# Performance work log

Hardware: AMD Instinct MI355X
Metric: run time of the kernel (lower is better)

## Reference

```python
import jax, jax.numpy as jnp
import numpy as np

B, S, D = 4, 2048, 1024
H = 2 * D          # hidden_dim = 2*n_embd
A = H // 16        # adapt_dim = 128
E = 8              # num_experts
K = 2              # top-k within group
GS = 4             # group_size
G = E // GS        # num_groups


def _ln(x, g, b, eps=1e-5):
    m = x.mean(-1, keepdims=True)
    v = x.var(-1, keepdims=True)
    return (x - m) / jnp.sqrt(v + eps) * g + b


def setup_inputs() -> dict:
    key = jax.random.key(0)
    ks = jax.random.split(key, 12)
    s = 1.0 / np.sqrt(D)       # shared MLP init scale
    sa = s * 0.01              # adapt layers init scale
    se = 0.01 / np.sqrt(A)     # expert adapter init scale
    f32 = jnp.float32
    return {
        "x": jax.random.normal(ks[0], (B, S, D), f32),
        "W_up": jax.random.normal(ks[1], (H, D), f32) * s,
        "W_gate": jax.random.normal(ks[2], (H, D), f32) * s,
        "W_down": jax.random.normal(ks[3], (D, H), f32) * s,
        "W_pre": jax.random.normal(ks[4], (A, D), f32) * sa,
        "W_post": jax.random.normal(ks[5], (A, H), f32) * sa,
        "g_an": jnp.ones((A,), f32),
        "b_an": jnp.zeros((A,), f32),
        "W_aproj": jax.random.normal(ks[6], (H, A), f32) * sa,
        "W_eadapt": jax.random.normal(ks[7], (E, A, A), f32) * se,
        "g_e": jnp.ones((E, A), f32),
        "b_e": jnp.zeros((E, A), f32),
        "W_eproj": jax.random.normal(ks[8], (H, A), f32) * se,
        "W_oproj": jax.random.normal(ks[9], (D, H), f32) * se,
        "W_rg": jax.random.normal(ks[10], (G, D), f32) * 0.001,
        "W_re": jax.random.normal(ks[11], (GS, D), f32) * 0.001,
    }


def reference(x, W_up, W_gate, W_down, W_pre, W_post, g_an, b_an, W_aproj,
              W_eadapt, g_e, b_e, W_eproj, W_oproj, W_rg, W_re):
    Bs, Ss, Ds = x.shape
    N = Bs * Ss
    xf = x.reshape(N, Ds)

    # ---- HierarchicalRouter ----
    gl = xf @ W_rg.T                                   # [N, G]
    gp = jax.nn.softmax(gl, axis=-1)
    gw = gp.max(axis=-1)                               # top-1 group weight
    gi = gp.argmax(axis=-1)                            # top-1 group index
    ll = xf @ W_re.T                                   # [N, GS]
    lp = jax.nn.softmax(ll, axis=-1)
    lw, li = jax.lax.top_k(lp, K)                      # [N, K]
    eidx = gi[:, None] * GS + li                       # global expert ids
    lw = lw / (lw.sum(-1, keepdims=True) + 1e-7)
    fw = gw[:, None] * lw                              # final weights [N, K]
    dispatch = jnp.zeros((N, E), x.dtype).at[jnp.arange(N)[:, None], eidx].set(fw)
    load = dispatch.sum(0)
    target = load.sum() / E
    load_balance_loss = jnp.mean((load - target) ** 2)
    z_loss = jnp.mean(gl ** 2) + jnp.mean(ll ** 2)
    router_loss = 0.001 * (load_balance_loss + z_loss)

    # ---- SharedExpertMLP ----
    up = x @ W_up.T                                    # [B, S, H]
    gate = x @ W_gate.T
    hidden = jax.nn.silu(gate) * up
    pre = x @ W_pre.T                                  # [B, S, A]
    a_in = _ln(pre, g_an, b_an)
    a_out = _ln(hidden @ W_post.T, g_an, b_an)
    aw = jax.nn.silu(jnp.clip(jnp.einsum('bsa,bta->bst', a_in, a_out), -5.0, 5.0))
    adapt = jnp.einsum('bst,bta->bsa', aw, a_in) @ W_aproj.T  # [B, S, H]
    hidden = hidden + 0.1 * adapt
    shared = hidden @ W_down.T                         # [B, S, D]

    # ---- ExpertGroup (vectorized gather/MLP/scatter) ----
    # sum_i w_i * (shared + 0.1*contrib_i) = shared*sum(w) + 0.1*sum_i w_i*contrib_i
    w = dispatch.reshape(Bs, Ss, E)                    # dispatch weights
    he = jnp.einsum('bsa,eca->ebsc', pre, W_eadapt)    # [E, B, S, A]
    he = _ln(he, g_e[:, None, None, :], b_e[:, None, None, :])
    wh = jnp.einsum('ebsa,bse->bsa', he, w)            # weighted combine at adapt_dim
    contrib = (wh @ W_eproj.T) @ W_oproj.T             # [B, S, D]
    out = shared * w.sum(-1, keepdims=True) + 0.1 * contrib
    return out, router_loss
```

## Files before the change

### kernel.cpp

```cpp
#include <hip/hip_runtime.h>
#include <hip/hip_bf16.h>

typedef unsigned short u16;
typedef short bf16x8 __attribute__((ext_vector_type(8)));
typedef float f32x4 __attribute__((ext_vector_type(4)));

#define N_TOK 8192
#define DIM   1024
#define HID   2048
#define ADIM  128
#define SEQ   2048
#define LDP   2304

__device__ __forceinline__ u16 f2bf_bits(float f){
  unsigned u = __float_as_uint(f);
  unsigned r = (u + 0x7fffu + ((u >> 16) & 1u)) >> 16;
  return (u16)r;
}
__device__ __forceinline__ float bf2f(u16 v){ return __uint_as_float((unsigned)v << 16); }
__device__ __forceinline__ float siluf(float x){ return x / (1.f + __expf(-x)); }

__device__ __forceinline__ void gload16(const void* g, void* l){
  __builtin_amdgcn_global_load_lds((const __attribute__((address_space(1))) void*)g,
                                   (__attribute__((address_space(3))) void*)l, 16, 0, 0);
// ... 129 lines not shown
      acc[2][n] = __builtin_amdgcn_mfma_f32_16x16x32_bf16(a[2], b[n], acc[2][n], 0, 0, 0);
    asm volatile("s_waitcnt lgkmcnt(0)" ::: "memory"); SB0();
    #pragma unroll
    for (int n = 0; n < 4; n++)
      acc[3][n] = __builtin_amdgcn_mfma_f32_16x16x32_bf16(a[3], b[n], acc[3][n], 0, 0, 0);
    __builtin_amdgcn_s_setprio(0);
    __builtin_amdgcn_s_barrier();

    a[0] = AFRAG(4, 1); SB0();
    a[1] = AFRAG(5, 1); SB0();
    a[2] = AFRAG(6, 1); SB0();
    a[3] = AFRAG(7, 1);
    stage(Wgu, bcol, ktn, 1, pn, 16384);
    __builtin_amdgcn_s_barrier();
    asm volatile("s_waitcnt lgkmcnt(3)" ::: "memory"); SB0();
    __builtin_amdgcn_s_setprio(1);
    #pragma unroll
    for (int n = 0; n < 4; n++)
      acc[4][n] = __builtin_amdgcn_mfma_f32_16x16x32_bf16(a[0], b[n], acc[4][n], 0, 0, 0);
    asm volatile("s_waitcnt lgkmcnt(2)" ::: "memory"); SB0();
    #pragma unroll
    for (int n = 0; n < 4; n++)
      acc[5][n] = __builtin_amdgcn_mfma_f32_16x16x32_bf16(a[1], b[n], acc[5][n], 0, 0, 0);
    asm volatile("s_waitcnt lgkmcnt(1)" ::: "memory"); SB0();
    #pragma unroll
    for (int n = 0; n < 4; n++)
      acc[6][n] = __builtin_amdgcn_mfma_f32_16x16x32_bf16(a[2], b[n], acc[6][n], 0, 0, 0);
    asm volatile("s_waitcnt lgkmcnt(0)" ::: "memory"); SB0();
    #pragma unroll
    for (int n = 0; n < 4; n++)
      acc[7][n] = __builtin_amdgcn_mfma_f32_16x16x32_bf16(a[3], b[n], acc[7][n], 0, 0, 0);
    __builtin_amdgcn_s_setprio(0);
    asm volatile("s_waitcnt vmcnt(4)" ::: "memory");
    __builtin_amdgcn_s_barrier();
  }
#undef AFRAG
#undef BFRAG

  #pragma unroll
  for (int mf = 0; mf < 8; mf++)
    #pragma unroll
    for (int i = 0; i < 4; i++) {
      const long r = brow + wm * 128 + mf * 16 + (lane >> 4) * 4 + i;
      const float sw = sumw[r];
      #pragma unroll
      for (int q = 0; q < 2; q++) {
        const float g = acc[mf][2 * q][i], u = acc[mf][2 * q + 1][i];
        const int hcol = (bn * 8 + wn * 2 + q) * 16 + (lane & 15);
        hidP[r * LDP + hcol] = f2bf_bits(sw * (siluf(g) * u));
      }
    }
}

enum { EPI_BF16 = 0, EPI_SILU = 2 };

template<int EPI>
__global__ void __launch_bounds__(256, 2)
gemm_bt(const u16* __restrict__ Ag, const u16* __restrict__ Bg, int K, int lda, int ldb,
        long sAz, long sBz, long sOz, u16* __restrict__ bout, int ldo, int col0)
{
  __shared__ u16 lA[128 * 32];
  __shared__ u16 lB[128 * 32];
  const int tid = threadIdx.x, wave = tid >> 6, lane = tid & 63;
  const long brow = (long)blockIdx.y * 128, bcol = (long)blockIdx.x * 128;
  const u16* A = Ag + (long)blockIdx.z * sAz + brow * lda;
  const u16* B = Bg + (long)blockIdx.z * sBz + bcol * ldb;
  const int wr = (wave >> 1) * 64, wc = (wave & 1) * 64;

  f32x4 acc[4][4];
  #pragma unroll
  for (int m = 0; m < 4; m++)
    #pragma unroll
    for (int n = 0; n < 4; n++)
      #pragma unroll
      for (int i = 0; i < 4; i++) acc[m][n][i] = 0.f;

  const int sr = tid >> 2, sks = ((tid & 3) ^ ((tid >> 3) & 3)) * 8;
  const u16* gA = A + (long)sr * lda + sks;
  const u16* gB = B + (long)sr * ldb + sks;
  const long rA = (long)64 * lda, rB = (long)64 * ldb;
  u16* lA0 = &lA[wave * 512]; u16* lA1 = &lA[2048 + wave * 512];
  u16* lB0 = &lB[wave * 512]; u16* lB1 = &lB[2048 + wave * 512];
  const int frow = lane & 15;
  const int fks = ((lane >> 4) * 8) ^ (((lane >> 1) & 3) << 3);

  for (int kt = 0; kt < K; kt += 32) {
    gload16(gA, lA0); gload16(gA + rA, lA1);
    gload16(gB, lB0); gload16(gB + rB, lB1);
    gA += 32; gB += 32;
    asm volatile("s_waitcnt vmcnt(0)" ::: "memory");
    __syncthreads();
    bf16x8 af[4], bfv[4];
    #pragma unroll
    for (int m = 0; m < 4; m++) af[m] = *(const bf16x8*)&lA[(wr + m * 16 + frow) * 32 + fks];
    #pragma unroll
    for (int n = 0; n < 4; n++) bfv[n] = *(const bf16x8*)&lB[(wc + n * 16 + frow) * 32 + fks];
    #pragma unroll
    for (int m = 0; m < 4; m++)
      #pragma unroll
      for (int n = 0; n < 4; n++)
        acc[m][n] = __builtin_amdgcn_mfma_f32_16x16x32_bf16(af[m], bfv[n], acc[m][n], 0, 0, 0);
    __syncthreads();
  }

  const long r0 = brow + wr + ((lane >> 4) << 2);
  const long c0 = bcol + wc + (lane & 15);
  u16* O = bout + (long)blockIdx.z * sOz;
  #pragma unroll
  for (int m = 0; m < 4; m++) {
    #pragma unroll
    for (int i = 0; i < 4; i++) {
      long r = r0 + m * 16 + i;
      #pragma unroll
      for (int n = 0; n < 4; n++) {
        long c = c0 + n * 16;
        float v = acc[m][n][i];
        if constexpr (EPI == EPI_BF16) {
          O[r * ldo + col0 + c] = f2bf_bits(v);
        } else {
          v = fminf(5.f, fmaxf(-5.f, v));
          O[r * ldo + c] = f2bf_bits(siluf(v));
        }
      }
    }
  }
}

__global__ void __launch_bounds__(256, 2)
gemm_f32(const u16* __restrict__ Ag, const u16* __restrict__ Bg,
         float* __restrict__ out)
{
  __shared__ u16 lA[128 * 32];
  __shared__ u16 lB[128 * 32];
  const int tid = threadIdx.x, wave = tid >> 6, lane = tid & 63;
  const long brow = (long)blockIdx.y * 128, bcol = (long)blockIdx.x * 128;
  const int wr = (wave >> 1) * 64, wc = (wave & 1) * 64;

  f32x4 acc[4][4];
  #pragma unroll
  for (int m = 0; m < 4; m++)
    #pragma unroll
    for (int n = 0; n < 4; n++)
      #pragma unroll
      for (int i = 0; i < 4; i++) acc[m][n][i] = 0.f;

  const int sr = tid >> 2, sks = ((tid & 3) ^ ((tid >> 3) & 3)) * 8;
  const u16* gA = Ag + brow * LDP + (long)sr * LDP + sks;
  const u16* gB = Bg + bcol * LDP + (long)sr * LDP + sks;
  const long rA = (long)64 * LDP, rB = (long)64 * LDP;
  u16* lA0 = &lA[wave * 512]; u16* lA1 = &lA[2048 + wave * 512];
  u16* lB0 = &lB[wave * 512]; u16* lB1 = &lB[2048 + wave * 512];
  const int frow = lane & 15;
  const int fks = ((lane >> 4) * 8) ^ (((lane >> 1) & 3) << 3);

  for (int kt = 0; kt < LDP; kt += 32) {
    gload16(gA, lA0); gload16(gA + rA, lA1);
    gload16(gB, lB0); gload16(gB + rB, lB1);
    gA += 32; gB += 32;
    asm volatile("s_waitcnt vmcnt(0)" ::: "memory");
    __syncthreads();
    bf16x8 af[4], bfv[4];
    #pragma unroll
    for (int m = 0; m < 4; m++) af[m] = *(const bf16x8*)&lA[(wr + m * 16 + frow) * 32 + fks];
    #pragma unroll
    for (int n = 0; n < 4; n++) bfv[n] = *(const bf16x8*)&lB[(wc + n * 16 + frow) * 32 + fks];
    #pragma unroll
    for (int m = 0; m < 4; m++)
      #pragma unroll
      for (int n = 0; n < 4; n++)
        acc[m][n] = __builtin_amdgcn_mfma_f32_16x16x32_bf16(af[m], bfv[n], acc[m][n], 0, 0, 0);
    __syncthreads();
  }

  const long r0 = brow + wr + ((lane >> 4) << 2);
  const long c0 = bcol + wc + (lane & 15);
  #pragma unroll
  for (int m = 0; m < 4; m++)
    #pragma unroll
    for (int i = 0; i < 4; i++) {
      long r = r0 + m * 16 + i;
      #pragma unroll
      for (int n = 0; n < 4; n++)
        out[r * DIM + c0 + n * 16] = acc[m][n][i];
    }
}

__global__ void __launch_bounds__(256, 2)
gemm_split(const u16* __restrict__ Ag, const u16* __restrict__ Bg, int Ksub, int nsplit,
           int lda, int ldb, long sAz, long sBz, float* __restrict__ part)
{
  __shared__ u16 lA[128 * 32];
  __shared__ u16 lB[128 * 32];
  const int tid = threadIdx.x, wave = tid >> 6, lane = tid & 63;
  const int z = blockIdx.z, batch = z / nsplit, split = z % nsplit;
  const long brow = (long)blockIdx.y * 128;
  const int Mrows = gridDim.y * 128;
  const u16* A = Ag + (long)batch * sAz + brow * lda + (long)split * Ksub;
  const u16* B = Bg + (long)batch * sBz + (long)split * Ksub;
  const int wr = (wave >> 1) * 64, wc = (wave & 1) * 64;

  f32x4 acc[4][4];
  #pragma unroll
  for (int m = 0; m < 4; m++)
    #pragma unroll
    for (int n = 0; n < 4; n++)
      #pragma unroll
      for (int i = 0; i < 4; i++) acc[m][n][i] = 0.f;

  const int sr = tid >> 2, sks = ((tid & 3) ^ ((tid >> 3) & 3)) * 8;
  const u16* gA = A + (long)sr * lda + sks;
  const u16* gB = B + (long)sr * ldb + sks;
  const long rA = (long)64 * lda, rB = (long)64 * ldb;
  u16* lA0 = &lA[wave * 512]; u16* lA1 = &lA[2048 + wave * 512];
  u16* lB0 = &lB[wave * 512]; u16* lB1 = &lB[2048 + wave * 512];
  const int frow = lane & 15;
  const int fks = ((lane >> 4) * 8) ^ (((lane >> 1) & 3) << 3);

  for (int kt = 0; kt < Ksub; kt += 32) {
    gload16(gA, lA0); gload16(gA + rA, lA1);
    gload16(gB, lB0); gload16(gB + rB, lB1);
    gA += 32; gB += 32;
    asm volatile("s_waitcnt vmcnt(0)" ::: "memory");
    __syncthreads();
    bf16x8 af[4], bfv[4];
    #pragma unroll
    for (int m = 0; m < 4; m++) af[m] = *(const bf16x8*)&lA[(wr + m * 16 + frow) * 32 + fks];
    #pragma unroll
    for (int n = 0; n < 4; n++) bfv[n] = *(const bf16x8*)&lB[(wc + n * 16 + frow) * 32 + fks];
    #pragma unroll
    for (int m = 0; m < 4; m++)
      #pragma unroll
      for (int n = 0; n < 4; n++)
        acc[m][n] = __builtin_amdgcn_mfma_f32_16x16x32_bf16(af[m], bfv[n], acc[m][n], 0, 0, 0);
    __syncthreads();
  }

  float* po = part + (long)z * Mrows * 128;
  const long rr = brow + wr + ((lane >> 4) << 2);
  const int cc = wc + (lane & 15);
  #pragma unroll
  for (int m = 0; m < 4; m++)
    #pragma unroll
    for (int i = 0; i < 4; i++) {
      long r = rr + m * 16 + i;
      #pragma unroll
      for (int n = 0; n < 4; n++)
        po[r * 128 + cc + n * 16] = acc[m][n][i];
    }
}

__global__ void __launch_bounds__(256, 2)
gemm_split_q(const u16* __restrict__ A0, const u16* __restrict__ B0, int lda0,
             const u16* __restrict__ A1, const u16* __restrict__ B1, int lda1,
             float* __restrict__ part)
{
  __shared__ u16 lA[128 * 32];
  __shared__ u16 lB[128 * 32];
  const int tid = threadIdx.x, wave = tid >> 6, lane = tid & 63;
  const int z = blockIdx.z, sel = z >> 2, split = z & 3;
  const long brow = (long)blockIdx.y * 128;
  const int lda = sel ? lda1 : lda0;
  const u16* A = (sel ? A1 : A0) + brow * lda + (long)split * 512;
  const u16* B = (sel ? B1 : B0) + (long)split * 512;

  const int wr = (wave >> 1) * 64, wc = (wave & 1) * 64;
  f32x4 acc[4][4];
  #pragma unroll
  for (int m = 0; m < 4; m++)
    #pragma unroll
    for (int n = 0; n < 4; n++)
      #pragma unroll
      for (int i = 0; i < 4; i++) acc[m][n][i] = 0.f;

  const int sr = tid >> 2, sks = ((tid & 3) ^ ((tid >> 3) & 3)) * 8;
  const u16* gA = A + (long)sr * lda + sks;
  const u16* gB = B + (long)sr * HID + sks;
  const long rA = (long)64 * lda, rB = (long)64 * HID;
  u16* lA0 = &lA[wave * 512]; u16* lA1 = &lA[2048 + wave * 512];
  u16* lB0 = &lB[wave * 512]; u16* lB1 = &lB[2048 + wave * 512];
  const int frow = lane & 15;
  const int fks = ((lane >> 4) * 8) ^ (((lane >> 1) & 3) << 3);

  for (int kt = 0; kt < 512; kt += 32) {
    gload16(gA, lA0); gload16(gA + rA, lA1);
    gload16(gB, lB0); gload16(gB + rB, lB1);
    gA += 32; gB += 32;
    asm volatile("s_waitcnt vmcnt(0)" ::: "memory");
    __syncthreads();
    bf16x8 af[4], bfv[4];
    #pragma unroll
    for (int m = 0; m < 4; m++) af[m] = *(const bf16x8*)&lA[(wr + m * 16 + frow) * 32 + fks];
    #pragma unroll
    for (int n = 0; n < 4; n++) bfv[n] = *(const bf16x8*)&lB[(wc + n * 16 + frow) * 32 + fks];
    #pragma unroll
    for (int m = 0; m < 4; m++)
      #pragma unroll
      for (int n = 0; n < 4; n++)
        acc[m][n] = __builtin_amdgcn_mfma_f32_16x16x32_bf16(af[m], bfv[n], acc[m][n], 0, 0, 0);
    __syncthreads();
  }

  float* po = part + (long)z * 131072;
  const long rr = brow + wr + ((lane >> 4) << 2);
  const int cc = wc + (lane & 15);
  #pragma unroll
  for (int m = 0; m < 4; m++)
    #pragma unroll
    for (int i = 0; i < 4; i++) {
      long r = rr + m * 16 + i;
      #pragma unroll
      for (int n = 0; n < 4; n++)
        po[r * 128 + cc + n * 16] = acc[m][n][i];
    }
}

__global__ void __launch_bounds__(256)
prep_all(const float* __restrict__ x, const float* __restrict__ Wrg,
         const float* __restrict__ Wre, float* __restrict__ sumw,
         float* __restrict__ fwv, int* __restrict__ eidxv,
         float* __restrict__ stats, u16* __restrict__ xb,
         const float* __restrict__ Wg, const float* __restrict__ Wu,
         const float* __restrict__ Wd, const float* __restrict__ Wo,
         const float* __restrict__ Wpost, const float* __restrict__ Wpre,
         const float* __restrict__ Wead,
         u16* __restrict__ Wgu, u16* __restrict__ WdQ,
         u16* __restrict__ Wob, u16* __restrict__ Wpostb,
         u16* __restrict__ Wpreb, u16* __restrict__ Weadb,
         const float* __restrict__ Wa, const float* __restrict__ We,
         u16* __restrict__ Ta, u16* __restrict__ Te)
{
  __shared__ float lst[10];
  const int blk = blockIdx.x;
  if (blk < 512) {
    if (threadIdx.x < 10) lst[threadIdx.x] = 0.f;
    __syncthreads();
    const int wave = threadIdx.x >> 6, lane = threadIdx.x & 63;
    const float4* wg0 = (const float4*)Wrg;
    const float4* wg1 = (const float4*)(Wrg + 1024);
    const float4* we0 = (const float4*)Wre;
    const float4* we1 = (const float4*)(Wre + 1024);
    const float4* we2 = (const float4*)(Wre + 2048);
    const float4* we3 = (const float4*)(Wre + 3072);
    for (int t = 0; t < 4; t++) {
      const long n = (long)blk * 16 + wave * 4 + t;
      const float4* xr = (const float4*)(x + n * 1024);
      float d0 = 0, d1 = 0, t0 = 0, t1 = 0, t2 = 0, t3 = 0;
      #pragma unroll
      for (int j = 0; j < 4; j++) {
        int id = j * 64 + lane;
        float4 xv = xr[id];
        ushort4 xc;
        xc.x = f2bf_bits(xv.x); xc.y = f2bf_bits(xv.y);
        xc.z = f2bf_bits(xv.z); xc.w = f2bf_bits(xv.w);
        *(ushort4*)(xb + n * 1024 + id * 4) = xc;
        float4 a;
        a = wg0[id]; d0 += xv.x * a.x + xv.y * a.y + xv.z * a.z + xv.w * a.w;
        a = wg1[id]; d1 += xv.x * a.x + xv.y * a.y + xv.z * a.z + xv.w * a.w;
        a = we0[id]; t0 += xv.x * a.x + xv.y * a.y + xv.z * a.z + xv.w * a.w;
        a = we1[id]; t1 += xv.x * a.x + xv.y * a.y + xv.z * a.z + xv.w * a.w;
        a = we2[id]; t2 += xv.x * a.x + xv.y * a.y + xv.z * a.z + xv.w * a.w;
        a = we3[id]; t3 += xv.x * a.x + xv.y * a.y + xv.z * a.z + xv.w * a.w;
      }
      #pragma unroll
      for (int o = 32; o; o >>= 1) {
        d0 += __shfl_xor(d0, o); d1 += __shfl_xor(d1, o);
        t0 += __shfl_xor(t0, o); t1 += __shfl_xor(t1, o);
// ... 19 lines not shown
        for (int i = 1; i < 4; i++) if (p[i] > p[i1]) i1 = i;
        int i2 = (i1 == 0) ? 1 : 0;
        #pragma unroll
        for (int i = 0; i < 4; i++) if (i != i1 && p[i] > p[i2]) i2 = i;
        float s2 = p[i1] + p[i2];
        float invs = 1.f / (s2 + 1e-7f);
        float f1 = gw * p[i1] * invs, f2 = gw * p[i2] * invs;
        int ea = gi * 4 + i1, eb = gi * 4 + i2;
        sumw[n] = f1 + f2;
        fwv[2 * n] = f1; fwv[2 * n + 1] = f2;
        eidxv[2 * n] = ea; eidxv[2 * n + 1] = eb;
        atomicAdd(&lst[ea], f1);
        atomicAdd(&lst[eb], f2);
        atomicAdd(&lst[8], d0 * d0 + d1 * d1);
        atomicAdd(&lst[9], t0 * t0 + t1 * t1 + t2 * t2 + t3 * t3);
      }
    }
    __syncthreads();
    if (threadIdx.x < 10) atomicAdd(&stats[threadIdx.x], lst[threadIdx.x]);
  } else if (blk < 4864) {
    long i = ((long)(blk - 512) * 256 + threadIdx.x) * 8;
    const float* s; u16* d; long so, doff;
    if (i < 4194304) {
      long rp = i >> 10, c = i & 1023;
      long i32 = rp >> 5, wi = rp & 31;
      s = (wi < 16) ? Wg : Wu;
      so = (i32 * 16 + (wi & 15)) * 1024 + c;
      d = Wgu; doff = i;
    } else if (i < 6291456) {
      long j = i - 4194304;
      long r = j >> 11, c = j & 2047;
      s = Wd; so = j;
      d = WdQ; doff = r * LDP + c;
    } else if (i < 8388608) { s = Wo;    so = i - 6291456; d = Wob;    doff = so; }
    else if (i < 8650752)   { s = Wpost; so = i - 8388608; d = Wpostb; doff = so; }
    else if (i < 8781824)   { s = Wpre;  so = i - 8650752; d = Wpreb;  doff = so; }
    else                    { s = Wead;  so = i - 8781824; d = Weadb;  doff = so; }
    float4 v0 = *(const float4*)(s + so), v1 = *(const float4*)(s + so + 4);
    ushort4 p, q;
    p.x = f2bf_bits(v0.x); p.y = f2bf_bits(v0.y); p.z = f2bf_bits(v0.z); p.w = f2bf_bits(v0.w);
    q.x = f2bf_bits(v1.x); q.y = f2bf_bits(v1.y); q.z = f2bf_bits(v1.z); q.w = f2bf_bits(v1.w);
    *(ushort4*)(d + doff) = p;
    *(ushort4*)(d + doff + 4) = q;
  } else {
    int bid = blk - 4864;
    const float* src = (bid < 1024) ? Wa : We;
    u16* dst = (bid < 1024) ? Ta : Te;
    int idx = (bid & 1023) * 256 + threadIdx.x;
    int c = idx >> 11, r = idx & 2047;
    dst[idx] = f2bf_bits(src[(long)r * 128 + c]);
  }
}

__global__ void reduce_q(const float* __restrict__ part, u16* __restrict__ WdQ)
{
  int idx = blockIdx.x * 256 + threadIdx.x;
  int r = idx >> 8, c = idx & 255;
  const float* p = part + ((c < 128) ? 0 : 524288) + (long)r * 128 + (c & 127);
  float a = p[0] + p[131072] + p[262144] + p[393216];
  WdQ[(long)r * LDP + 2048 + c] = f2bf_bits(a);
}

__global__ void __launch_bounds__(256)
ln_rows_part(const float* __restrict__ part, int nsplit,
             const float* __restrict__ g, const float* __restrict__ b,
             const float* __restrict__ sumw,
             u16* __restrict__ out, u16* __restrict__ outT, u16* __restrict__ rawout)
{
  int wave = threadIdx.x >> 6, lane = threadIdx.x & 63;
  long n = (long)blockIdx.x * 4 + wave;
  long base = n * 128;
  float x0 = 0.f, x1 = 0.f;
  for (int s = 0; s < nsplit; s++) {
    x0 += part[(long)s * (N_TOK * ADIM) + base + lane];
    x1 += part[(long)s * (N_TOK * ADIM) + base + 64 + lane];
  }
  if (sumw) { float inv = 1.f / sumw[n]; x0 *= inv; x1 *= inv; }
  float s2 = x0 + x1, q = x0 * x0 + x1 * x1;
  #pragma unroll
  for (int o = 32; o; o >>= 1) { s2 += __shfl_xor(s2, o); q += __shfl_xor(q, o); }
  float m = s2 * (1.f / 128.f);
  float var = q * (1.f / 128.f) - m * m;
  float inv = rsqrtf(var + 1e-5f);
  float y0 = (x0 - m) * inv * g[lane] + b[lane];
  float y1 = (x1 - m) * inv * g[lane + 64] + b[lane + 64];
  out[base + lane] = f2bf_bits(y0);
  out[base + 64 + lane] = f2bf_bits(y1);
  if (outT) {
    long bb = n >> 11, ss = n & 2047;
    outT[(bb * 128 + lane) * 2048 + ss] = f2bf_bits(y0);
    outT[(bb * 128 + lane + 64) * 2048 + ss] = f2bf_bits(y1);
  }
  if (rawout) {
    rawout[base + lane] = f2bf_bits(x0);
    rawout[base + 64 + lane] = f2bf_bits(x1);
  }
}

__global__ void reduce_part_p1(const float* __restrict__ part,
                               const float* __restrict__ sumw, u16* __restrict__ hidP)
{
  int idx = blockIdx.x * 256 + threadIdx.x;
  int n = idx >> 5, c4 = (idx & 31) * 4;
  int batch = n >> 11, r = n & 2047;
  float4 a = {0.f, 0.f, 0.f, 0.f};
  #pragma unroll
  for (int s = 0; s < 4; s++) {
    float4 v = *(const float4*)(part + (((long)(batch * 4 + s) * 2048 + r) << 7) + c4);
    a.x += v.x; a.y += v.y; a.z += v.z; a.w += v.w;
  }
  float rs = 0.1f * sumw[n];
  ushort4 o;
  o.x = f2bf_bits(rs * a.x); o.y = f2bf_bits(rs * a.y);
  o.z = f2bf_bits(rs * a.z); o.w = f2bf_bits(rs * a.w);
  *(ushort4*)(hidP + (long)n * LDP + 2048 + c4) = o;
}

__global__ void init_stats(float* stats){ if (threadIdx.x < 16) stats[threadIdx.x] = 0.f; }

__global__ void finalize_loss(const float* __restrict__ stats, float* __restrict__ out)
{
  float tot = 0;
  #pragma unroll
  for (int e = 0; e < 8; e++) tot += stats[e];
  float target = tot * 0.125f;
  float lb = 0;
  #pragma unroll
  for (int e = 0; e < 8; e++) { float d = stats[e] - target; lb += d * d; }
  lb *= 0.125f;
  float z = stats[8] * (1.f / (8192.f * 2.f)) + stats[9] * (1.f / (8192.f * 4.f));
  out[0] = 0.001f * (lb + z);
}

__global__ void __launch_bounds__(256)
ln_combine(const u16* __restrict__ he, const int* __restrict__ eidxv,
           const float* __restrict__ fwv, const float* __restrict__ g_e,
           const float* __restrict__ b_e, u16* __restrict__ hidP)
{
  const int wave = threadIdx.x >> 6, lane = threadIdx.x & 63;
  const long n = (long)blockIdx.x * 4 + wave;
  float o0 = 0.f, o1 = 0.f;
  #pragma unroll
  for (int k = 0; k < 2; k++) {
    const int e = eidxv[2 * n + k];
    const float w = fwv[2 * n + k];
    const u16* row = he + ((long)e * N_TOK + n) * 128;
    float h0 = bf2f(row[lane]), h1 = bf2f(row[lane + 64]);
    float s = h0 + h1, q = h0 * h0 + h1 * h1;
    #pragma unroll
    for (int o = 32; o; o >>= 1) { s += __shfl_xor(s, o); q += __shfl_xor(q, o); }
    float m = s * (1.f / 128.f);
    float var = q * (1.f / 128.f) - m * m;
    float inv = rsqrtf(var + 1e-5f);
    o0 += w * ((h0 - m) * inv * g_e[e * 128 + lane] + b_e[e * 128 + lane]);
    o1 += w * ((h1 - m) * inv * g_e[e * 128 + lane + 64] + b_e[e * 128 + lane + 64]);
  }
  hidP[n * LDP + 2176 + lane] = f2bf_bits(0.1f * o0);
  hidP[n * LDP + 2176 + 64 + lane] = f2bf_bits(0.1f * o1);
}

extern "C" void kernel_launch(void* const* d_in, const int* in_sizes, int n_in,
                              void* d_out, int out_size, void* d_ws, size_t ws_size,
                              hipStream_t stream)
{
  (void)in_sizes; (void)n_in; (void)out_size; (void)ws_size;
  const float* x       = (const float*)d_in[0];
  const float* W_up    = (const float*)d_in[1];
  const float* W_gate  = (const float*)d_in[2];
  const float* W_down  = (const float*)d_in[3];
  const float* W_pre   = (const float*)d_in[4];
  const float* W_post  = (const float*)d_in[5];
  const float* g_an    = (const float*)d_in[6];
  const float* b_an    = (const float*)d_in[7];
  const float* W_aproj = (const float*)d_in[8];
  const float* W_ead   = (const float*)d_in[9];
  const float* g_e     = (const float*)d_in[10];
  const float* b_e     = (const float*)d_in[11];
  const float* W_eproj = (const float*)d_in[12];
  const float* W_oproj = (const float*)d_in[13];
  const float* W_rg    = (const float*)d_in[14];
  const float* W_re    = (const float*)d_in[15];
  float* out = (float*)d_out;

  char* base = (char*)d_ws; size_t off = 0;
  auto alloc = [&](size_t bytes) -> void* {
    void* p = base + off; off = (off + bytes + 255) & ~(size_t)255; return p;
  };
  u16*   xb     = (u16*)  alloc((size_t)N_TOK * DIM * 2);
  u16*   Wgu    = (u16*)  alloc((size_t)2 * HID * DIM * 2);
  u16*   WdQ    = (u16*)  alloc((size_t)DIM * LDP * 2);
  u16*   Wob    = (u16*)  alloc((size_t)DIM * HID * 2);
  u16*   Wpostb = (u16*)  alloc((size_t)ADIM * HID * 2);
  u16*   Wpreb  = (u16*)  alloc((size_t)ADIM * DIM * 2);
  u16*   WaTb   = (u16*)  alloc((size_t)ADIM * HID * 2);
  u16*   WeTb   = (u16*)  alloc((size_t)ADIM * HID * 2);
  u16*   Weadb  = (u16*)  alloc((size_t)8 * ADIM * ADIM * 2);
  u16*   hidP   = (u16*)  alloc((size_t)N_TOK * LDP * 2);
  u16*   heb    = (u16*)  alloc((size_t)8 * N_TOK * ADIM * 2);
  float* part   = (float*)heb;
  u16*   preb   = (u16*)  alloc((size_t)N_TOK * ADIM * 2);
  u16*   a_in   = (u16*)  alloc((size_t)N_TOK * ADIM * 2);
  u16*   a_inT  = (u16*)  alloc((size_t)N_TOK * ADIM * 2);
  u16*   a_out  = (u16*)  alloc((size_t)N_TOK * ADIM * 2);
  float* sumw   = (float*)alloc((size_t)N_TOK * 4);
  float* fwv    = (float*)alloc((size_t)N_TOK * 2 * 4);
  int*   eidxv  = (int*)  alloc((size_t)N_TOK * 2 * 4);
  float* stats  = (float*)alloc(64);
  u16* aw = (u16*)d_out;

  hipFuncSetAttribute((const void*)gemm_gu256,
                      hipFuncAttributeMaxDynamicSharedMemorySize, 131072);

  init_stats<<<1, 64, 0, stream>>>(stats);

  prep_all<<<6912, 256, 0, stream>>>(x, W_rg, W_re, sumw, fwv, eidxv, stats, xb,
                                     W_gate, W_up, W_down, W_oproj, W_post, W_pre,
                                     W_ead, Wgu, WdQ, Wob, Wpostb, Wpreb, Weadb,
                                     W_aproj, W_eproj, WaTb, WeTb);

  gemm_split_q<<<dim3(1, 8, 8), 256, 0, stream>>>(WdQ, WaTb, LDP, Wob, WeTb, HID, part);
  reduce_q<<<1024, 256, 0, stream>>>(part, WdQ);

  gemm_gu256<<<512, 512, 131072, stream>>>(xb, Wgu, sumw, hidP);

  gemm_split<<<dim3(1, 64, 4), 256, 0, stream>>>(xb, Wpreb, 256, 4, DIM, DIM, 0, 0, part);
  ln_rows_part<<<2048, 256, 0, stream>>>(part, 4, g_an, b_an, nullptr, a_in, a_inT, preb);

  gemm_bt<EPI_BF16><<<dim3(1, 64, 8), 256, 0, stream>>>(preb, Weadb, ADIM, ADIM, ADIM,
      0, (long)ADIM * ADIM, (long)N_TOK * ADIM, heb, ADIM, 0);
  ln_combine<<<2048, 256, 0, stream>>>(heb, eidxv, fwv, g_e, b_e, hidP);

  gemm_split<<<dim3(1, 64, 4), 256, 0, stream>>>(hidP, Wpostb, 512, 4, LDP, HID, 0, 0, part);
  ln_rows_part<<<2048, 256, 0, stream>>>(part, 4, g_an, b_an, sumw, a_out, nullptr, nullptr);

  gemm_bt<EPI_SILU><<<dim3(16, 16, 4), 256, 0, stream>>>(a_in, a_out, ADIM, ADIM, ADIM,
      (long)SEQ * ADIM, (long)SEQ * ADIM, (long)SEQ * SEQ, aw, SEQ, 0);

  gemm_split<<<dim3(1, 16, 16), 256, 0, stream>>>(aw, a_inT, 512, 4, SEQ, SEQ,
      (long)SEQ * SEQ, (long)ADIM * SEQ, part);
  reduce_part_p1<<<1024, 256, 0, stream>>>(part, sumw, hidP);

  gemm_f32<<<dim3(8, 64, 1), 256, 0, stream>>>(hidP, WdQ, out);

  finalize_loss<<<1, 1, 0, stream>>>(stats, out + (size_t)N_TOK * DIM);
}
```

Before: 269.9 us.

## Merge independent GEMM and layernorm launches into fewer combined kernels

Small independent GEMMs and their follow-up reductions and layernorms now share launches, dispatched by block-index ranges. The pre-projection GEMM runs with the weight-fold GEMM, the expert-adapter GEMM with the post-projection GEMM, and their layernorm or reduce steps are paired the same way. Loss finalisation moves into the last GEMM, and the stats init becomes a memset. This cuts launch count and tail underutilisation from small grids, at the cost of reusing the output buffer as scratch for partial sums.

```diff
diff --git a/kernel.cpp b/kernel.cpp
--- a/kernel.cpp
+++ b/kernel.cpp
@@ -205,29 +205,12 @@
     }
 }
 
-enum { EPI_BF16 = 0, EPI_SILU = 2 };
-
-template<int EPI>
-__global__ void __launch_bounds__(256, 2)
-gemm_bt(const u16* __restrict__ Ag, const u16* __restrict__ Bg, int K, int lda, int ldb,
-        long sAz, long sBz, long sOz, u16* __restrict__ bout, int ldo, int col0)
-{
-  __shared__ u16 lA[128 * 32];
-  __shared__ u16 lB[128 * 32];
+__device__ __forceinline__ void kloop128(const u16* __restrict__ A, const u16* __restrict__ B,
+                                         int lda, int ldb, int K,
+                                         u16* lA, u16* lB, f32x4 (&acc)[4][4])
+{
   const int tid = threadIdx.x, wave = tid >> 6, lane = tid & 63;
-  const long brow = (long)blockIdx.y * 128, bcol = (long)blockIdx.x * 128;
-  const u16* A = Ag + (long)blockIdx.z * sAz + brow * lda;
-  const u16* B = Bg + (long)blockIdx.z * sBz + bcol * ldb;
   const int wr = (wave >> 1) * 64, wc = (wave & 1) * 64;
-
-  f32x4 acc[4][4];
-  #pragma unroll
-  for (int m = 0; m < 4; m++)
-    #pragma unroll
-    for (int n = 0; n < 4; n++)
-      #pragma unroll
-      for (int i = 0; i < 4; i++) acc[m][n][i] = 0.f;
-
   const int sr = tid >> 2, sks = ((tid & 3) ^ ((tid >> 3) & 3)) * 8;
   const u16* gA = A + (long)sr * lda + sks;
   const u16* gB = B + (long)sr * ldb + sks;
@@ -255,76 +238,193 @@
         acc[m][n] = __builtin_amdgcn_mfma_f32_16x16x32_bf16(af[m], bfv[n], acc[m][n], 0, 0, 0);
     __syncthreads();
   }
-
+}
+
+__device__ __forceinline__ void acc_zero(f32x4 (&acc)[4][4]){
+  #pragma unroll
+  for (int m = 0; m < 4; m++)
+    #pragma unroll
+    for (int n = 0; n < 4; n++)
+      #pragma unroll
+      for (int i = 0; i < 4; i++) acc[m][n][i] = 0.f;
+}
+
+__global__ void __launch_bounds__(256, 2)
+gemm_silu(const u16* __restrict__ Ag, const u16* __restrict__ Bg,
+          u16* __restrict__ bout)
+{
+  __shared__ u16 lA[4096];
+  __shared__ u16 lB[4096];
+  const int wave = threadIdx.x >> 6, lane = threadIdx.x & 63;
+  const long brow = (long)blockIdx.y * 128, bcol = (long)blockIdx.x * 128;
+  const u16* A = Ag + (long)blockIdx.z * (SEQ * ADIM) + brow * ADIM;
+  const u16* B = Bg + (long)blockIdx.z * (SEQ * ADIM) + bcol * ADIM;
+  f32x4 acc[4][4]; acc_zero(acc);
+  kloop128(A, B, ADIM, ADIM, ADIM, lA, lB, acc);
+  const int wr = (wave >> 1) * 64, wc = (wave & 1) * 64;
   const long r0 = brow + wr + ((lane >> 4) << 2);
   const long c0 = bcol + wc + (lane & 15);
-  u16* O = bout + (long)blockIdx.z * sOz;
+  u16* O = bout + (long)blockIdx.z * ((long)SEQ * SEQ);
   #pragma unroll
-  for (int m = 0; m < 4; m++) {
+  for (int m = 0; m < 4; m++)
     #pragma unroll
     for (int i = 0; i < 4; i++) {
       long r = r0 + m * 16 + i;
       #pragma unroll
       for (int n = 0; n < 4; n++) {
-        long c = c0 + n * 16;
         float v = acc[m][n][i];
-        if constexpr (EPI == EPI_BF16) {
-          O[r * ldo + col0 + c] = f2bf_bits(v);
-        } else {
-          v = fminf(5.f, fmaxf(-5.f, v));
-          O[r * ldo + c] = f2bf_bits(siluf(v));
-        }
-      }
-    }
+        v = fminf(5.f, fmaxf(-5.f, v));
+        O[r * SEQ + c0 + n * 16] = f2bf_bits(siluf(v));
+      }
+    }
+}
+
+__global__ void __launch_bounds__(256, 2)
+gemm_split_p1(const u16* __restrict__ aw, const u16* __restrict__ a_inT,
+              float* __restrict__ part)
+{
+  __shared__ u16 lA[4096];
+  __shared__ u16 lB[4096];
+  const int wave = threadIdx.x >> 6, lane = threadIdx.x & 63;
+  const int z = blockIdx.z, batch = z >> 2, split = z & 3;
+  const long brow = (long)blockIdx.y * 128;
+  const u16* A = aw + (long)batch * SEQ * SEQ + brow * SEQ + (long)split * 512;
+  const u16* B = a_inT + (long)batch * ADIM * SEQ + (long)split * 512;
+  f32x4 acc[4][4]; acc_zero(acc);
+  kloop128(A, B, SEQ, SEQ, 512, lA, lB, acc);
+  float* po = part + (long)z * (SEQ * ADIM);
+  const int wr = (wave >> 1) * 64, wc = (wave & 1) * 64;
+  const long rr = brow + wr + ((lane >> 4) << 2);
+  const int cc = wc + (lane & 15);
+  #pragma unroll
+  for (int m = 0; m < 4; m++)
+    #pragma unroll
+    for (int i = 0; i < 4; i++) {
+      long r = rr + m * 16 + i;
+      #pragma unroll
+      for (int n = 0; n < 4; n++)
+        po[r * 128 + cc + n * 16] = acc[m][n][i];
+    }
+}
+
+__global__ void __launch_bounds__(256, 2)
+split_pq(const u16* __restrict__ xb, const u16* __restrict__ Wpreb,
+         const u16* __restrict__ WdQ, const u16* __restrict__ WaTb,
+         const u16* __restrict__ Wob, const u16* __restrict__ WeTb,
+         float* __restrict__ part, float* __restrict__ qpart)
+{
+  __shared__ u16 lA[4096];
+  __shared__ u16 lB[4096];
+  const int blk = blockIdx.x;
+  const int wave = threadIdx.x >> 6, lane = threadIdx.x & 63;
+  f32x4 acc[4][4]; acc_zero(acc);
+  const int wr = (wave >> 1) * 64, wc = (wave & 1) * 64;
+
+  if (blk < 256) {
+    const int y = blk & 63, z = blk >> 6;
+    const long brow = (long)y * 128;
+    const u16* A = xb + brow * DIM + (long)z * 256;
+    const u16* B = Wpreb + (long)z * 256;
+    kloop128(A, B, DIM, DIM, 256, lA, lB, acc);
+    float* po = part + (long)z * (N_TOK * ADIM);
+    const long rr = brow + wr + ((lane >> 4) << 2);
+    const int cc = wc + (lane & 15);
+    #pragma unroll
+    for (int m = 0; m < 4; m++)
+      #pragma unroll
+      for (int i = 0; i < 4; i++) {
+        long r = rr + m * 16 + i;
+        #pragma unroll
+        for (int n = 0; n < 4; n++)
+          po[r * 128 + cc + n * 16] = acc[m][n][i];
+      }
+  } else {
+    const int q = blk - 256;
+    const int y = q & 7, z = q >> 3;
+    const int sel = z >> 2, split = z & 3;
+    const long brow = (long)y * 128;
+    const int lda = sel ? HID : LDP;
+    const u16* A = (sel ? Wob : WdQ) + brow * lda + (long)split * 512;
+    const u16* B = (sel ? WeTb : WaTb) + (long)split * 512;
+    kloop128(A, B, lda, HID, 512, lA, lB, acc);
+    float* po = qpart + (long)z * 131072;
+    const long rr = brow + wr + ((lane >> 4) << 2);
+    const int cc = wc + (lane & 15);
+    #pragma unroll
+    for (int m = 0; m < 4; m++)
+      #pragma unroll
+      for (int i = 0; i < 4; i++) {
+        long r = rr + m * 16 + i;
+        #pragma unroll
+        for (int n = 0; n < 4; n++)
+          po[r * 128 + cc + n * 16] = acc[m][n][i];
+      }
+  }
+}
+
+__global__ void __launch_bounds__(256, 2)
+he_postf(const u16* __restrict__ preb, const u16* __restrict__ Weadb,
+         u16* __restrict__ heb, const u16* __restrict__ hidP,
+         const u16* __restrict__ Wpostb, float* __restrict__ postfp)
+{
+  __shared__ u16 lA[4096];
+  __shared__ u16 lB[4096];
+  const int blk = blockIdx.x;
+  const int wave = threadIdx.x >> 6, lane = threadIdx.x & 63;
+  f32x4 acc[4][4]; acc_zero(acc);
+  const int wr = (wave >> 1) * 64, wc = (wave & 1) * 64;
+
+  if (blk < 512) {
+    const int y = blk & 63, e = blk >> 6;
+    const long brow = (long)y * 128;
+    const u16* A = preb + brow * ADIM;
+    const u16* B = Weadb + (long)e * ADIM * ADIM;
+    kloop128(A, B, ADIM, ADIM, ADIM, lA, lB, acc);
+    u16* O = heb + (long)e * N_TOK * ADIM;
+    const long r0 = brow + wr + ((lane >> 4) << 2);
+    const long c0 = wc + (lane & 15);
+    #pragma unroll
+    for (int m = 0; m < 4; m++)
+      #pragma unroll
+      for (int i = 0; i < 4; i++) {
+        long r = r0 + m * 16 + i;
+        #pragma unroll
+        for (int n = 0; n < 4; n++)
+          O[r * ADIM + c0 + n * 16] = f2bf_bits(acc[m][n][i]);
+      }
+  } else {
+    const int q = blk - 512;
+    const int y = q & 63, z = q >> 6;
+    const long brow = (long)y * 128;
+    const u16* A = hidP + brow * LDP + (long)z * 512;
+    const u16* B = Wpostb + (long)z * 512;
+    kloop128(A, B, LDP, HID, 512, lA, lB, acc);
+    float* po = postfp + (long)z * (N_TOK * ADIM);
+    const long rr = brow + wr + ((lane >> 4) << 2);
+    const int cc = wc + (lane & 15);
+    #pragma unroll
+    for (int m = 0; m < 4; m++)
+      #pragma unroll
+      for (int i = 0; i < 4; i++) {
+        long r = rr + m * 16 + i;
+        #pragma unroll
+        for (int n = 0; n < 4; n++)
+          po[r * 128 + cc + n * 16] = acc[m][n][i];
+      }
   }
 }
 
 __global__ void __launch_bounds__(256, 2)
 gemm_f32(const u16* __restrict__ Ag, const u16* __restrict__ Bg,
-         float* __restrict__ out)
-{
-  __shared__ u16 lA[128 * 32];
-  __shared__ u16 lB[128 * 32];
-  const int tid = threadIdx.x, wave = tid >> 6, lane = tid & 63;
+         const float* __restrict__ stats, float* __restrict__ out)
+{
+  __shared__ u16 lA[4096];
+  __shared__ u16 lB[4096];
+  const int wave = threadIdx.x >> 6, lane = threadIdx.x & 63;
   const long brow = (long)blockIdx.y * 128, bcol = (long)blockIdx.x * 128;
+  f32x4 acc[4][4]; acc_zero(acc);
+  kloop128(Ag + brow * LDP, Bg + bcol * LDP, LDP, LDP, LDP, lA, lB, acc);
   const int wr = (wave >> 1) * 64, wc = (wave & 1) * 64;
-
-  f32x4 acc[4][4];
-  #pragma unroll
-  for (int m = 0; m < 4; m++)
-    #pragma unroll
-    for (int n = 0; n < 4; n++)
-      #pragma unroll
-      for (int i = 0; i < 4; i++) acc[m][n][i] = 0.f;
-
-  const int sr = tid >> 2, sks = ((tid & 3) ^ ((tid >> 3) & 3)) * 8;
-  const u16* gA = Ag + brow * LDP + (long)sr * LDP + sks;
-  const u16* gB = Bg + bcol * LDP + (long)sr * LDP + sks;
-  const long rA = (long)64 * LDP, rB = (long)64 * LDP;
-  u16* lA0 = &lA[wave * 512]; u16* lA1 = &lA[2048 + wave * 512];
-  u16* lB0 = &lB[wave * 512]; u16* lB1 = &lB[2048 + wave * 512];
-  const int frow = lane & 15;
-  const int fks = ((lane >> 4) * 8) ^ (((lane >> 1) & 3) << 3);
-
-  for (int kt = 0; kt < LDP; kt += 32) {
-    gload16(gA, lA0); gload16(gA + rA, lA1);
-    gload16(gB, lB0); gload16(gB + rB, lB1);
-    gA += 32; gB += 32;
-    asm volatile("s_waitcnt vmcnt(0)" ::: "memory");
-    __syncthreads();
-    bf16x8 af[4], bfv[4];
-    #pragma unroll
-    for (int m = 0; m < 4; m++) af[m] = *(const bf16x8*)&lA[(wr + m * 16 + frow) * 32 + fks];
-    #pragma unroll
-    for (int n = 0; n < 4; n++) bfv[n] = *(const bf16x8*)&lB[(wc + n * 16 + frow) * 32 + fks];
-    #pragma unroll
-    for (int m = 0; m < 4; m++)
-      #pragma unroll
-      for (int n = 0; n < 4; n++)
-        acc[m][n] = __builtin_amdgcn_mfma_f32_16x16x32_bf16(af[m], bfv[n], acc[m][n], 0, 0, 0);
-    __syncthreads();
-  }
-
   const long r0 = brow + wr + ((lane >> 4) << 2);
   const long c0 = bcol + wc + (lane & 15);
   #pragma unroll
@@ -336,135 +436,18 @@
       for (int n = 0; n < 4; n++)
         out[r * DIM + c0 + n * 16] = acc[m][n][i];
     }
-}
-
-__global__ void __launch_bounds__(256, 2)
-gemm_split(const u16* __restrict__ Ag, const u16* __restrict__ Bg, int Ksub, int nsplit,
-           int lda, int ldb, long sAz, long sBz, float* __restrict__ part)
-{
-  __shared__ u16 lA[128 * 32];
-  __shared__ u16 lB[128 * 32];
-  const int tid = threadIdx.x, wave = tid >> 6, lane = tid & 63;
-  const int z = blockIdx.z, batch = z / nsplit, split = z % nsplit;
-  const long brow = (long)blockIdx.y * 128;
-  const int Mrows = gridDim.y * 128;
-  const u16* A = Ag + (long)batch * sAz + brow * lda + (long)split * Ksub;
-  const u16* B = Bg + (long)batch * sBz + (long)split * Ksub;
-  const int wr = (wave >> 1) * 64, wc = (wave & 1) * 64;
-
-  f32x4 acc[4][4];
-  #pragma unroll
-  for (int m = 0; m < 4; m++)
-    #pragma unroll
-    for (int n = 0; n < 4; n++)
-      #pragma unroll
-      for (int i = 0; i < 4; i++) acc[m][n][i] = 0.f;
-
-  const int sr = tid >> 2, sks = ((tid & 3) ^ ((tid >> 3) & 3)) * 8;
-  const u16* gA = A + (long)sr * lda + sks;
-  const u16* gB = B + (long)sr * ldb + sks;
-  const long rA = (long)64 * lda, rB = (long)64 * ldb;
-  u16* lA0 = &lA[wave * 512]; u16* lA1 = &lA[2048 + wave * 512];
-  u16* lB0 = &lB[wave * 512]; u16* lB1 = &lB[2048 + wave * 512];
-  const int frow = lane & 15;
-  const int fks = ((lane >> 4) * 8) ^ (((lane >> 1) & 3) << 3);
-
-  for (int kt = 0; kt < Ksub; kt += 32) {
-    gload16(gA, lA0); gload16(gA + rA, lA1);
-    gload16(gB, lB0); gload16(gB + rB, lB1);
-    gA += 32; gB += 32;
-    asm volatile("s_waitcnt vmcnt(0)" ::: "memory");
-    __syncthreads();
-    bf16x8 af[4], bfv[4];
-    #pragma unroll
-    for (int m = 0; m < 4; m++) af[m] = *(const bf16x8*)&lA[(wr + m * 16 + frow) * 32 + fks];
-    #pragma unroll
-    for (int n = 0; n < 4; n++) bfv[n] = *(const bf16x8*)&lB[(wc + n * 16 + frow) * 32 + fks];
-    #pragma unroll
-    for (int m = 0; m < 4; m++)
-      #pragma unroll
-      for (int n = 0; n < 4; n++)
-        acc[m][n] = __builtin_amdgcn_mfma_f32_16x16x32_bf16(af[m], bfv[n], acc[m][n], 0, 0, 0);
-    __syncthreads();
-  }
-
-  float* po = part + (long)z * Mrows * 128;
-  const long rr = brow + wr + ((lane >> 4) << 2);
-  const int cc = wc + (lane & 15);
-  #pragma unroll
-  for (int m = 0; m < 4; m++)
-    #pragma unroll
-    for (int i = 0; i < 4; i++) {
-      long r = rr + m * 16 + i;
-      #pragma unroll
-      for (int n = 0; n < 4; n++)
-        po[r * 128 + cc + n * 16] = acc[m][n][i];
-    }
-}
-
-__global__ void __launch_bounds__(256, 2)
-gemm_split_q(const u16* __restrict__ A0, const u16* __restrict__ B0, int lda0,
-             const u16* __restrict__ A1, const u16* __restrict__ B1, int lda1,
-             float* __restrict__ part)
-{
-  __shared__ u16 lA[128 * 32];
-  __shared__ u16 lB[128 * 32];
-  const int tid = threadIdx.x, wave = tid >> 6, lane = tid & 63;
-  const int z = blockIdx.z, sel = z >> 2, split = z & 3;
-  const long brow = (long)blockIdx.y * 128;
-  const int lda = sel ? lda1 : lda0;
-  const u16* A = (sel ? A1 : A0) + brow * lda + (long)split * 512;
-  const u16* B = (sel ? B1 : B0) + (long)split * 512;
-
-  const int wr = (wave >> 1) * 64, wc = (wave & 1) * 64;
-  f32x4 acc[4][4];
-  #pragma unroll
-  for (int m = 0; m < 4; m++)
-    #pragma unroll
-    for (int n = 0; n < 4; n++)
-      #pragma unroll
-      for (int i = 0; i < 4; i++) acc[m][n][i] = 0.f;
-
-  const int sr = tid >> 2, sks = ((tid & 3) ^ ((tid >> 3) & 3)) * 8;
-  const u16* gA = A + (long)sr * lda + sks;
-  const u16* gB = B + (long)sr * HID + sks;
-  const long rA = (long)64 * lda, rB = (long)64 * HID;
-  u16* lA0 = &lA[wave * 512]; u16* lA1 = &lA[2048 + wave * 512];
-  u16* lB0 = &lB[wave * 512]; u16* lB1 = &lB[2048 + wave * 512];
-  const int frow = lane & 15;
-  const int fks = ((lane >> 4) * 8) ^ (((lane >> 1) & 3) << 3);
-
-  for (int kt = 0; kt < 512; kt += 32) {
-    gload16(gA, lA0); gload16(gA + rA, lA1);
-    gload16(gB, lB0); gload16(gB + rB, lB1);
-    gA += 32; gB += 32;
-    asm volatile("s_waitcnt vmcnt(0)" ::: "memory");
-    __syncthreads();
-    bf16x8 af[4], bfv[4];
-    #pragma unroll
-    for (int m = 0; m < 4; m++) af[m] = *(const bf16x8*)&lA[(wr + m * 16 + frow) * 32 + fks];
-    #pragma unroll
-    for (int n = 0; n < 4; n++) bfv[n] = *(const bf16x8*)&lB[(wc + n * 16 + frow) * 32 + fks];
-    #pragma unroll
-    for (int m = 0; m < 4; m++)
-      #pragma unroll
-      for (int n = 0; n < 4; n++)
-        acc[m][n] = __builtin_amdgcn_mfma_f32_16x16x32_bf16(af[m], bfv[n], acc[m][n], 0, 0, 0);
-    __syncthreads();
-  }
-
-  float* po = part + (long)z * 131072;
-  const long rr = brow + wr + ((lane >> 4) << 2);
-  const int cc = wc + (lane & 15);
-  #pragma unroll
-  for (int m = 0; m < 4; m++)
-    #pragma unroll
-    for (int i = 0; i < 4; i++) {
-      long r = rr + m * 16 + i;
-      #pragma unroll
-      for (int n = 0; n < 4; n++)
-        po[r * 128 + cc + n * 16] = acc[m][n][i];
-    }
+  if (blockIdx.x == 0 && blockIdx.y == 0 && threadIdx.x == 0) {
+    float tot = 0;
+    #pragma unroll
+    for (int e = 0; e < 8; e++) tot += stats[e];
+    float target = tot * 0.125f;
+    float lb = 0;
+    #pragma unroll
+    for (int e = 0; e < 8; e++) { float d = stats[e] - target; lb += d * d; }
+    lb *= 0.125f;
+    float z = stats[8] * (1.f / (8192.f * 2.f)) + stats[9] * (1.f / (8192.f * 4.f));
+    out[(size_t)N_TOK * DIM] = 0.001f * (lb + z);
+  }
 }
 
 __global__ void __launch_bounds__(256)
@@ -590,48 +573,95 @@
   }
 }
 
-__global__ void reduce_q(const float* __restrict__ part, u16* __restrict__ WdQ)
-{
-  int idx = blockIdx.x * 256 + threadIdx.x;
-  int r = idx >> 8, c = idx & 255;
-  const float* p = part + ((c < 128) ? 0 : 524288) + (long)r * 128 + (c & 127);
-  float a = p[0] + p[131072] + p[262144] + p[393216];
-  WdQ[(long)r * LDP + 2048 + c] = f2bf_bits(a);
-}
-
 __global__ void __launch_bounds__(256)
-ln_rows_part(const float* __restrict__ part, int nsplit,
-             const float* __restrict__ g, const float* __restrict__ b,
-             const float* __restrict__ sumw,
-             u16* __restrict__ out, u16* __restrict__ outT, u16* __restrict__ rawout)
-{
-  int wave = threadIdx.x >> 6, lane = threadIdx.x & 63;
-  long n = (long)blockIdx.x * 4 + wave;
-  long base = n * 128;
-  float x0 = 0.f, x1 = 0.f;
-  for (int s = 0; s < nsplit; s++) {
-    x0 += part[(long)s * (N_TOK * ADIM) + base + lane];
-    x1 += part[(long)s * (N_TOK * ADIM) + base + 64 + lane];
-  }
-  if (sumw) { float inv = 1.f / sumw[n]; x0 *= inv; x1 *= inv; }
-  float s2 = x0 + x1, q = x0 * x0 + x1 * x1;
-  #pragma unroll
-  for (int o = 32; o; o >>= 1) { s2 += __shfl_xor(s2, o); q += __shfl_xor(q, o); }
-  float m = s2 * (1.f / 128.f);
-  float var = q * (1.f / 128.f) - m * m;
-  float inv = rsqrtf(var + 1e-5f);
-  float y0 = (x0 - m) * inv * g[lane] + b[lane];
-  float y1 = (x1 - m) * inv * g[lane + 64] + b[lane + 64];
-  out[base + lane] = f2bf_bits(y0);
-  out[base + 64 + lane] = f2bf_bits(y1);
-  if (outT) {
+ln1_rq(const float* __restrict__ part, const float* __restrict__ qpart,
+       const float* __restrict__ g, const float* __restrict__ b,
+       u16* __restrict__ a_in, u16* __restrict__ a_inT, u16* __restrict__ preb,
+       u16* __restrict__ WdQ)
+{
+  const int blk = blockIdx.x;
+  if (blk < 2048) {
+    int wave = threadIdx.x >> 6, lane = threadIdx.x & 63;
+    long n = (long)blk * 4 + wave;
+    long base = n * 128;
+    float x0 = 0.f, x1 = 0.f;
+    #pragma unroll
+    for (int s = 0; s < 4; s++) {
+      x0 += part[(long)s * (N_TOK * ADIM) + base + lane];
+      x1 += part[(long)s * (N_TOK * ADIM) + base + 64 + lane];
+    }
+    float s2 = x0 + x1, q = x0 * x0 + x1 * x1;
+    #pragma unroll
+    for (int o = 32; o; o >>= 1) { s2 += __shfl_xor(s2, o); q += __shfl_xor(q, o); }
+    float m = s2 * (1.f / 128.f);
+    float var = q * (1.f / 128.f) - m * m;
+    float inv = rsqrtf(var + 1e-5f);
+    float y0 = (x0 - m) * inv * g[lane] + b[lane];
+    float y1 = (x1 - m) * inv * g[lane + 64] + b[lane + 64];
+    a_in[base + lane] = f2bf_bits(y0);
+    a_in[base + 64 + lane] = f2bf_bits(y1);
     long bb = n >> 11, ss = n & 2047;
-    outT[(bb * 128 + lane) * 2048 + ss] = f2bf_bits(y0);
-    outT[(bb * 128 + lane + 64) * 2048 + ss] = f2bf_bits(y1);
-  }
-  if (rawout) {
-    rawout[base + lane] = f2bf_bits(x0);
-    rawout[base + 64 + lane] = f2bf_bits(x1);
+    a_inT[(bb * 128 + lane) * 2048 + ss] = f2bf_bits(y0);
+    a_inT[(bb * 128 + lane + 64) * 2048 + ss] = f2bf_bits(y1);
+    preb[base + lane] = f2bf_bits(x0);
+    preb[base + 64 + lane] = f2bf_bits(x1);
+  } else {
+    int idx = (blk - 2048) * 256 + threadIdx.x;
+    int r = idx >> 8, c = idx & 255;
+    const float* p = qpart + ((c < 128) ? 0 : 524288) + (long)r * 128 + (c & 127);
+    float a = p[0] + p[131072] + p[262144] + p[393216];
+    WdQ[(long)r * LDP + 2048 + c] = f2bf_bits(a);
+  }
+}
+
+__global__ void __launch_bounds__(256)
+lnc_ln2(const u16* __restrict__ heb, const int* __restrict__ eidxv,
+        const float* __restrict__ fwv, const float* __restrict__ g_e,
+        const float* __restrict__ b_e, u16* __restrict__ hidP,
+        const float* __restrict__ postfp, const float* __restrict__ g_an,
+        const float* __restrict__ b_an, const float* __restrict__ sumw,
+        u16* __restrict__ a_out)
+{
+  const int blk = blockIdx.x;
+  const int wave = threadIdx.x >> 6, lane = threadIdx.x & 63;
+  if (blk < 2048) {
+    const long n = (long)blk * 4 + wave;
+    float o0 = 0.f, o1 = 0.f;
+    #pragma unroll
+    for (int k = 0; k < 2; k++) {
+      const int e = eidxv[2 * n + k];
+      const float w = fwv[2 * n + k];
+      const u16* row = heb + ((long)e * N_TOK + n) * 128;
+      float h0 = bf2f(row[lane]), h1 = bf2f(row[lane + 64]);
+      float s = h0 + h1, q = h0 * h0 + h1 * h1;
+      #pragma unroll
+      for (int o = 32; o; o >>= 1) { s += __shfl_xor(s, o); q += __shfl_xor(q, o); }
+      float m = s * (1.f / 128.f);
+      float var = q * (1.f / 128.f) - m * m;
+      float inv = rsqrtf(var + 1e-5f);
+      o0 += w * ((h0 - m) * inv * g_e[e * 128 + lane] + b_e[e * 128 + lane]);
+      o1 += w * ((h1 - m) * inv * g_e[e * 128 + lane + 64] + b_e[e * 128 + lane + 64]);
+    }
+    hidP[n * LDP + 2176 + lane] = f2bf_bits(0.1f * o0);
+    hidP[n * LDP + 2176 + 64 + lane] = f2bf_bits(0.1f * o1);
+  } else {
+    long n = (long)(blk - 2048) * 4 + wave;
+    long base = n * 128;
+    float x0 = 0.f, x1 = 0.f;
+    #pragma unroll
+    for (int s = 0; s < 4; s++) {
+      x0 += postfp[(long)s * (N_TOK * ADIM) + base + lane];
+      x1 += postfp[(long)s * (N_TOK * ADIM) + base + 64 + lane];
+    }
+    float invw = 1.f / sumw[n]; x0 *= invw; x1 *= invw;
+    float s2 = x0 + x1, q = x0 * x0 + x1 * x1;
+    #pragma unroll
+    for (int o = 32; o; o >>= 1) { s2 += __shfl_xor(s2, o); q += __shfl_xor(q, o); }
+    float m = s2 * (1.f / 128.f);
+    float var = q * (1.f / 128.f) - m * m;
+    float inv = rsqrtf(var + 1e-5f);
+    a_out[base + lane] = f2bf_bits((x0 - m) * inv * g_an[lane] + b_an[lane]);
+    a_out[base + 64 + lane] = f2bf_bits((x1 - m) * inv * g_an[lane + 64] + b_an[lane + 64]);
   }
 }
 
@@ -652,49 +682,6 @@
   o.x = f2bf_bits(rs * a.x); o.y = f2bf_bits(rs * a.y);
   o.z = f2bf_bits(rs * a.z); o.w = f2bf_bits(rs * a.w);
   *(ushort4*)(hidP + (long)n * LDP + 2048 + c4) = o;
-}
-
-__global__ void init_stats(float* stats){ if (threadIdx.x < 16) stats[threadIdx.x] = 0.f; }
-
-__global__ void finalize_loss(const float* __restrict__ stats, float* __restrict__ out)
-{
-  float tot = 0;
-  #pragma unroll
-  for (int e = 0; e < 8; e++) tot += stats[e];
-  float target = tot * 0.125f;
-  float lb = 0;
-  #pragma unroll
-  for (int e = 0; e < 8; e++) { float d = stats[e] - target; lb += d * d; }
-  lb *= 0.125f;
-  float z = stats[8] * (1.f / (8192.f * 2.f)) + stats[9] * (1.f / (8192.f * 4.f));
-  out[0] = 0.001f * (lb + z);
-}
-
-__global__ void __launch_bounds__(256)
-ln_combine(const u16* __restrict__ he, const int* __restrict__ eidxv,
-           const float* __restrict__ fwv, const float* __restrict__ g_e,
-           const float* __restrict__ b_e, u16* __restrict__ hidP)
-{
-  const int wave = threadIdx.x >> 6, lane = threadIdx.x & 63;
-  const long n = (long)blockIdx.x * 4 + wave;
-  float o0 = 0.f, o1 = 0.f;
-  #pragma unroll
-  for (int k = 0; k < 2; k++) {
-    const int e = eidxv[2 * n + k];
-    const float w = fwv[2 * n + k];
-    const u16* row = he + ((long)e * N_TOK + n) * 128;
-    float h0 = bf2f(row[lane]), h1 = bf2f(row[lane + 64]);
-    float s = h0 + h1, q = h0 * h0 + h1 * h1;
-    #pragma unroll
-    for (int o = 32; o; o >>= 1) { s += __shfl_xor(s, o); q += __shfl_xor(q, o); }
-    float m = s * (1.f / 128.f);
-    float var = q * (1.f / 128.f) - m * m;
-    float inv = rsqrtf(var + 1e-5f);
-    o0 += w * ((h0 - m) * inv * g_e[e * 128 + lane] + b_e[e * 128 + lane]);
-    o1 += w * ((h1 - m) * inv * g_e[e * 128 + lane + 64] + b_e[e * 128 + lane + 64]);
-  }
-  hidP[n * LDP + 2176 + lane] = f2bf_bits(0.1f * o0);
-  hidP[n * LDP + 2176 + 64 + lane] = f2bf_bits(0.1f * o1);
 }
 
 extern "C" void kernel_launch(void* const* d_in, const int* in_sizes, int n_in,
@@ -744,41 +731,36 @@
   float* fwv    = (float*)alloc((size_t)N_TOK * 2 * 4);
   int*   eidxv  = (int*)  alloc((size_t)N_TOK * 2 * 4);
   float* stats  = (float*)alloc(64);
-  u16* aw = (u16*)d_out;
+  float* postfp = (float*)d_out;
+  float* qpart  = (float*)((char*)d_out + 16777216);
+  u16*   aw     = (u16*)d_out;
 
   hipFuncSetAttribute((const void*)gemm_gu256,
                       hipFuncAttributeMaxDynamicSharedMemorySize, 131072);
 
-  init_stats<<<1, 64, 0, stream>>>(stats);
+  hipMemsetAsync(stats, 0, 64, stream);
 
   prep_all<<<6912, 256, 0, stream>>>(x, W_rg, W_re, sumw, fwv, eidxv, stats, xb,
                                      W_gate, W_up, W_down, W_oproj, W_post, W_pre,
                                      W_ead, Wgu, WdQ, Wob, Wpostb, Wpreb, Weadb,
                                      W_aproj, W_eproj, WaTb, WeTb);
 
-  gemm_split_q<<<dim3(1, 8, 8), 256, 0, stream>>>(WdQ, WaTb, LDP, Wob, WeTb, HID, part);
-  reduce_q<<<1024, 256, 0, stream>>>(part, WdQ);
-
   gemm_gu256<<<512, 512, 131072, stream>>>(xb, Wgu, sumw, hidP);
 
-  gemm_split<<<dim3(1, 64, 4), 256, 0, stream>>>(xb, Wpreb, 256, 4, DIM, DIM, 0, 0, part);
-  ln_rows_part<<<2048, 256, 0, stream>>>(part, 4, g_an, b_an, nullptr, a_in, a_inT, preb);
-
-  gemm_bt<EPI_BF16><<<dim3(1, 64, 8), 256, 0, stream>>>(preb, Weadb, ADIM, ADIM, ADIM,
-      0, (long)ADIM * ADIM, (long)N_TOK * ADIM, heb, ADIM, 0);
-  ln_combine<<<2048, 256, 0, stream>>>(heb, eidxv, fwv, g_e, b_e, hidP);
-
-  gemm_split<<<dim3(1, 64, 4), 256, 0, stream>>>(hidP, Wpostb, 512, 4, LDP, HID, 0, 0, part);
-  ln_rows_part<<<2048, 256, 0, stream>>>(part, 4, g_an, b_an, sumw, a_out, nullptr, nullptr);
-
-  gemm_bt<EPI_SILU><<<dim3(16, 16, 4), 256, 0, stream>>>(a_in, a_out, ADIM, ADIM, ADIM,
-      (long)SEQ * ADIM, (long)SEQ * ADIM, (long)SEQ * SEQ, aw, SEQ, 0);
-
-  gemm_split<<<dim3(1, 16, 16), 256, 0, stream>>>(aw, a_inT, 512, 4, SEQ, SEQ,
-      (long)SEQ * SEQ, (long)ADIM * SEQ, part);
+  split_pq<<<320, 256, 0, stream>>>(xb, Wpreb, WdQ, WaTb, Wob, WeTb, part, qpart);
+
+  ln1_rq<<<3072, 256, 0, stream>>>(part, qpart, g_an, b_an, a_in, a_inT, preb, WdQ);
+
+  he_postf<<<768, 256, 0, stream>>>(preb, Weadb, heb, hidP, Wpostb, postfp);
+
+  lnc_ln2<<<4096, 256, 0, stream>>>(heb, eidxv, fwv, g_e, b_e, hidP,
+                                    postfp, g_an, b_an, sumw, a_out);
+
+  gemm_silu<<<dim3(16, 16, 4), 256, 0, stream>>>(a_in, a_out, aw);
+
+  gemm_split_p1<<<dim3(1, 16, 16), 256, 0, stream>>>(aw, a_inT, part);
+
   reduce_part_p1<<<1024, 256, 0, stream>>>(part, sumw, hidP);
 
-  gemm_f32<<<dim3(8, 64, 1), 256, 0, stream>>>(hidP, WdQ, out);
-
-  finalize_loss<<<1, 1, 0, stream>>>(stats, out + (size_t)N_TOK * DIM);
-}
+  gemm_f32<<<dim3(8, 64, 1), 256, 0, stream>>>(hidP, WdQ, stats, out);
+}
```

Measured after the change: 243.4 us. 9.8% less time.
